# Kernel optimization log

Measured on AMD Instinct MI355X. Metric: run time of the kernel, lower is better.

## Reference

```python
import jax, jax.numpy as jnp
import numpy as np

N = 50000      # nodes
E = 600000     # edges
G = 256        # graphs in batch
HID = 128      # gcn hidden = gcn in = gcn out
EDIM = 16      # edge feature dim
EH = 64        # edge mlp hidden
NL = 4         # gcn layers
MIN_ = 200     # mol feature dim
MH = 256       # mlp hidden
MOUT = 128     # mlp out
PH = 512       # predictor hidden
PIN = HID + MOUT


def setup_inputs() -> dict:
    key = jax.random.key(0)
    ks = jax.random.split(key, 32)
    f = lambda k, s: jax.random.normal(k, s, dtype=jnp.float32)
    p = lambda k, s: 0.05 * jax.random.normal(k, s, dtype=jnp.float32)
    return {
        "x": f(ks[0], (N, HID)),
        "edge_index": jax.random.randint(ks[1], (2, E), 0, N),
        "edge_attr": f(ks[2], (E, EDIM)),
        "batch_index": jnp.sort(jax.random.randint(ks[3], (N,), 0, G)),
        "mol_features": f(ks[4], (G, MIN_)),
        # PDNConv params (stacked over NL layers)
        "conv_lin_W": p(ks[5], (NL, HID, HID)),
        "conv_mW1": p(ks[6], (NL, EDIM, EH)),
        "conv_mb1": p(ks[7], (NL, EH)),
        "conv_mW2": p(ks[8], (NL, EH)),
        "conv_mb2": p(ks[9], (NL,)),
        "conv_bias": p(ks[10], (NL, HID)),
        # dense Linear after each conv
        "gcn_W": p(ks[11], (NL, HID, HID)),
        "gcn_b": p(ks[12], (NL, HID)),
        # mol-feature MLP (n_mlp_layers=3 -> 4 linears)
        "mlp_W0": p(ks[13], (MIN_, MH)), "mlp_b0": p(ks[14], (MH,)),
        "mlp_W1": p(ks[15], (MH, MH)),   "mlp_b1": p(ks[16], (MH,)),
        "mlp_W2": p(ks[17], (MH, MH)),   "mlp_b2": p(ks[18], (MH,)),
        "mlp_W3": p(ks[19], (MH, MOUT)), "mlp_b3": p(ks[20], (MOUT,)),
        # predictor
        "pred_W0": p(ks[21], (PIN, PH)), "pred_b0": p(ks[22], (PH,)),
        "pred_W1": p(ks[23], (PH, PH)),  "pred_b1": p(ks[24], (PH,)),
        "out_W": p(ks[25], (PH, 1)),     "out_b": p(ks[26], (1,)),
    }


def _pdn_conv(h, row, col, edge_attr, lin_W, mW1, mb1, mW2, mb2, bias):
    # edge MLP -> sigmoid gate (PyG PDNConv)
    w = jax.nn.sigmoid(jnp.maximum(edge_attr @ mW1 + mb1, 0.0) @ mW2 + mb2)  # [E]
    # gcn_norm with self loops (fill weight 1.0)
    loop = jnp.arange(N)
    r = jnp.concatenate([row, loop])
    c = jnp.concatenate([col, loop])
    w_all = jnp.concatenate([w, jnp.ones((N,), h.dtype)])
    deg = jax.ops.segment_sum(w_all, c, num_segments=N)
    dinv = jnp.where(deg > 0, jax.lax.rsqrt(deg), 0.0)
    norm = dinv[r] * w_all * dinv[c]                                          # [E+N]
    hl = h @ lin_W                                                            # [N,HID]
    out = jax.ops.segment_sum(norm[:, None] * hl[r], c, num_segments=N)
    return out + bias


def reference(x, edge_index, edge_attr, batch_index, mol_features,
              conv_lin_W, conv_mW1, conv_mb1, conv_mW2, conv_mb2, conv_bias,
              gcn_W, gcn_b,
              mlp_W0, mlp_b0, mlp_W1, mlp_b1, mlp_W2, mlp_b2, mlp_W3, mlp_b3,
              pred_W0, pred_b0, pred_W1, pred_b1, out_W, out_b):
    row, col = edge_index[0], edge_index[1]
    relu = lambda v: jnp.maximum(v, 0.0)

    # GCN stack: PDNConv -> relu(Linear), x NL
    h1 = x
    for i in range(NL):
        h1 = _pdn_conv(h1, row, col, edge_attr, conv_lin_W[i], conv_mW1[i],
                       conv_mb1[i], conv_mW2[i], conv_mb2[i], conv_bias[i])
        h1 = relu(h1 @ gcn_W[i] + gcn_b[i])
    # global mean pool over graphs
    sums = jax.ops.segment_sum(h1, batch_index, num_segments=G)
    cnts = jax.ops.segment_sum(jnp.ones((N,), h1.dtype), batch_index, num_segments=G)
    h1 = sums / jnp.maximum(cnts, 1.0)[:, None]                               # [G,HID]

    # molecular-feature MLP
    h2 = relu(mol_features @ mlp_W0 + mlp_b0)
    h2 = relu(h2 @ mlp_W1 + mlp_b1)
    h2 = relu(h2 @ mlp_W2 + mlp_b2)
    h2 = relu(h2 @ mlp_W3 + mlp_b3)                                           # [G,MOUT]

    h = jnp.concatenate([h1, h2], axis=1)                                     # [G,PIN]
    h = relu(h @ pred_W0 + pred_b0)
    h = relu(h @ pred_W1 + pred_b1)
    return h @ out_W + out_b                                                  # [G,1]
```

## Files before the change

### kernel.cpp

```cpp
#include <hip/hip_runtime.h>
#include <hip/hip_bf16.h>


#define NN 50000
#define EE 600000
#define GG 256
#define HID 128
#define EDIM 16
#define EHID 64
#define NL 4
#define MIN_F 200
#define MH 256
#define MOUT 128
#define PH 512
#define PIN 256
#define SCAN_B 196
#define PCH 8
#define EMB 128

typedef __hip_bfloat16 bf16;
typedef __attribute__((ext_vector_type(8))) short bf16x8;
typedef __attribute__((ext_vector_type(4))) float f32x4;

__device__ __forceinline__ float bfl(unsigned u) { return __uint_as_float(u << 16); }
__device__ __forceinline__ float bfh(unsigned u) { return __uint_as_float(u & 0xffff0000u); }
__device__ __forceinline__ float b2f(bf16 x) { return __bfloat162float(x); }
__device__ __forceinline__ float ldf(const void* p, long i, bool bf) {
  return bf ? __bfloat162float(((const bf16*)p)[i]) : ((const float*)p)[i];
}
__device__ __forceinline__ unsigned short f2bf_bits(float v) {
  bf16 h = __float2bfloat16(v);
  return *reinterpret_cast<unsigned short*>(&h);
}

__global__ void probe_kernel(const unsigned short* __restrict__ xs, int* flag) {
  if (threadIdx.x == 0 && blockIdx.x == 0) {
    int sane = 0;
    for (int i = 0; i < 128; i++) {
      unsigned e = (xs[i] >> 7) & 0xFF;
      if (e >= 96 && e <= 159) sane++;
    }
    *flag = (sane >= 112) ? 1 : 0;
  }
}

__global__ __launch_bounds__(256) void cvt_to_bf16(const void* __restrict__ in,
                                                   unsigned short* __restrict__ outp,
                                                   int n8, const int* __restrict__ flag) {
  bool bf = *flag != 0;
  int i = blockIdx.x * 256 + threadIdx.x;
  if (i >= n8) return;
  if (bf) {
    reinterpret_cast<uint4*>(outp)[i] = reinterpret_cast<const uint4*>(in)[i];
  } else {
    const float4* p = reinterpret_cast<const float4*>(in) + (size_t)i * 2;
    float4 v0 = p[0], v1 = p[1];
    ushort4 a, b;
    a.x = f2bf_bits(v0.x); a.y = f2bf_bits(v0.y);
    a.z = f2bf_bits(v0.z); a.w = f2bf_bits(v0.w);
    b.x = f2bf_bits(v1.x); b.y = f2bf_bits(v1.y);
    b.z = f2bf_bits(v1.z); b.w = f2bf_bits(v1.w);
    reinterpret_cast<ushort4*>(outp)[i * 2] = a;
    reinterpret_cast<ushort4*>(outp)[i * 2 + 1] = b;
  }
}

__global__ __launch_bounds__(256) void cvt_molf(const void* __restrict__ in,
                                                float* __restrict__ outp,
                                                const int* __restrict__ flag) {
  bool bf = *flag != 0;
  int i = blockIdx.x * 256 + threadIdx.x;
  if (i >= GG * 50) return;
  int row = i / 50, c4 = (i % 50) * 4;
  float4 v;
  if (bf) {
    const unsigned short* p = (const unsigned short*)in + (size_t)row * MIN_F + c4;
    uint2 u = *reinterpret_cast<const uint2*>(p);
    v.x = bfl(u.x); v.y = bfh(u.x); v.z = bfl(u.y); v.w = bfh(u.y);
  } else {
    v = *reinterpret_cast<const float4*>((const float*)in + (size_t)row * MIN_F + c4);
  }
  *reinterpret_cast<float4*>(&outp[(size_t)row * 256 + c4]) = v;
}

__global__ __launch_bounds__(256) void prep_fused_w(const void* __restrict__ lin_W,
                                                    const void* __restrict__ gW,
                                                    unsigned short* __restrict__ Wt,
                                                    const int* __restrict__ flag) {
  bool bf = *flag != 0;
  int idx = blockIdx.x * 256 + threadIdx.x;
  if (idx >= 4 * 16384) return;
  int l = idx >> 14;
  int rem = idx & 16383;
  int n = rem >> 7, k = rem & 127;
  float s = 0.f;
  long lb = (long)l * 16384;
  for (int m = 0; m < 128; m++)
    s += ldf(lin_W, lb + (long)k * 128 + m, bf) * ldf(gW, lb + (long)m * 128 + n, bf);
  Wt[idx] = f2bf_bits(s);
}

__global__ __launch_bounds__(128) void prep_fused_b(const void* __restrict__ cbias,
                                                    const void* __restrict__ gW,
                                                    const void* __restrict__ gb,
                                                    float* __restrict__ bprime,
                                                    const int* __restrict__ flag) {
  bool bf = *flag != 0;
  int idx = blockIdx.x * 128 + threadIdx.x;
  if (idx >= NL * HID) return;
  int l = idx >> 7, n = idx & 127;
  float s = ldf(gb, idx, bf);
  long lb = (long)l * 16384;
  for (int k = 0; k < 128; k++)
    s += ldf(cbias, (long)l * 128 + k, bf) * ldf(gW, lb + (long)k * 128 + n, bf);
  bprime[idx] = s;
}

__global__ __launch_bounds__(256) void prep_edge_w(const void* __restrict__ mW1,
                                                   const void* __restrict__ mb1,
                                                   unsigned short* __restrict__ W1t,
                                                   const int* __restrict__ flag) {
  bool bf = *flag != 0;
  int idx = blockIdx.x * 256 + threadIdx.x;
  if (idx >= 256 * 32) return;
  int col = idx >> 5, k = idx & 31;
  float v = 0.f;
  if (k < EDIM) v = ldf(mW1, (long)(col >> 6) * (EDIM * EHID) + (long)k * EHID + (col & 63), bf);
  else if (k == EDIM) v = ldf(mb1, col, bf);
  W1t[idx] = f2bf_bits(v);
}

__global__ __launch_bounds__(256) void prep_tail(
    const void* __restrict__ mlpW0, const void* __restrict__ mlpW1,
    const void* __restrict__ mlpW2, const void* __restrict__ mlpW3,
    const void* __restrict__ predW0, const void* __restrict__ predW1,
    unsigned short* __restrict__ T, const int* __restrict__ flag) {
  bool bf = *flag != 0;
  int idx = blockIdx.x * 256 + threadIdx.x;
  const void* src; int N, Kp, Ksrc, off;
  if      (idx < 65536)  { src = mlpW0;  N = 256; Kp = 256; Ksrc = 200; off = 0; }
  else if (idx < 131072) { src = mlpW1;  N = 256; Kp = 256; Ksrc = 256; off = 65536; }
  else if (idx < 196608) { src = mlpW2;  N = 256; Kp = 256; Ksrc = 256; off = 131072; }
  else if (idx < 229376) { src = mlpW3;  N = 128; Kp = 256; Ksrc = 256; off = 196608; }
  else if (idx < 360448) { src = predW0; N = 512; Kp = 256; Ksrc = 256; off = 229376; }
  else if (idx < 622592) { src = predW1; N = 512; Kp = 512; Ksrc = 512; off = 360448; }
  else return;
  int rem = idx - off;
  int n = rem / Kp, k = rem % Kp;
  float v = (k < Ksrc) ? ldf(src, (long)k * N + n, bf) : 0.f;
  T[idx] = f2bf_bits(v);
}

__global__ __launch_bounds__(256) void count_kernel(const int* __restrict__ ei,
                                                    int* __restrict__ cnt) {
  int e = blockIdx.x * 256 + threadIdx.x;
  if (e >= EE) return;
  int c = ei[EE + e];
  c = min(max(c, 0), NN - 1);
  atomicAdd(&cnt[c], 1);
}

__global__ __launch_bounds__(256) void scan_phase1(const int* __restrict__ cnt,
                                                   int* __restrict__ bsum) {
  __shared__ int red[256];
  int tid = threadIdx.x;
  int i = blockIdx.x * 256 + tid;
  red[tid] = (i < NN) ? cnt[i] : 0;
  __syncthreads();
  for (int off = 128; off > 0; off >>= 1) {
    if (tid < off) red[tid] += red[tid + off];
    __syncthreads();
  }
  if (tid == 0) bsum[blockIdx.x] = red[0];
}

__global__ __launch_bounds__(256) void scan_phase2(int* __restrict__ bsum,
                                                   int* __restrict__ offs) {
  __shared__ int buf[256];
  int tid = threadIdx.x;
  int v = (tid < SCAN_B) ? bsum[tid] : 0;
  buf[tid] = v;
  __syncthreads();
  for (int off = 1; off < 256; off <<= 1) {
    int t = (tid >= off) ? buf[tid - off] : 0;
    __syncthreads();
    buf[tid] += t;
    __syncthreads();
  }
  if (tid < SCAN_B) bsum[tid] = buf[tid] - v;
  if (tid == 255) offs[NN] = buf[255];
}

__global__ __launch_bounds__(256) void scan_phase3(const int* __restrict__ cnt,
                                                   const int* __restrict__ bsum,
                                                   int* __restrict__ offs) {
  __shared__ int buf[256];
  int tid = threadIdx.x;
  int i = blockIdx.x * 256 + tid;
  int v = (i < NN) ? cnt[i] : 0;
  buf[tid] = v;
  __syncthreads();
  for (int off = 1; off < 256; off <<= 1) {
    int t = (tid >= off) ? buf[tid - off] : 0;
    __syncthreads();
    buf[tid] += t;
    __syncthreads();
  }
  if (i < NN) offs[i] = bsum[blockIdx.x] + buf[tid] - v;
}

__global__ __launch_bounds__(256) void fill_kernel(const int* __restrict__ ei,
                                                   const int* __restrict__ offs,
                                                   int* __restrict__ cursor,
                                                   int2* __restrict__ csr_se) {
  int e = blockIdx.x * 256 + threadIdx.x;
  if (e >= EE) return;
  int c = ei[EE + e];
  c = min(max(c, 0), NN - 1);
  int pos = offs[c] + atomicAdd(&cursor[c], 1);
  pos = min(max(pos, 0), EE - 1);
  csr_se[pos] = make_int2(ei[e], e);
}

__global__ __launch_bounds__(256) void edge_mlp_mfma(
    const void* __restrict__ eattr, const unsigned short* __restrict__ W1t,
    const void* __restrict__ mW2, const void* __restrict__ mb2,
    float* __restrict__ w_all4, const int* __restrict__ flag) {
  bool bf = *flag != 0;
  int tid = threadIdx.x;
  int wave = tid >> 6, lane = tid & 63;
  int l15 = lane & 15, quad = lane >> 4;

  bf16x8 afrag[4];
#pragma unroll
  for (int t = 0; t < 4; t++)
    afrag[t] =
        *reinterpret_cast<const bf16x8*>(&W1t[((wave * 4 + t) * 16 + l15) * 32 + quad * 8]);

  float w2v[16];
#pragma unroll
  for (int t = 0; t < 4; t++)
#pragma unroll
    for (int r = 0; r < 4; r++)
      w2v[t * 4 + r] = ldf(mW2, wave * 64 + t * 16 + quad * 4 + r, bf);
  float b2 = ldf(mb2, wave, bf);

  bf16x8 bconst = (bf16x8){0, 0, 0, 0, 0, 0, 0, 0};
  if (quad == 2) bconst[0] = (short)0x3F80;

  int ebase = blockIdx.x * EMB;
  int rowbytes = bf ? EDIM * 2 : EDIM * 4;
  const char* p = (const char*)eattr + (size_t)(ebase + l15) * rowbytes +
                  (size_t)quad * (rowbytes >> 1);
  int fragstep = 16 * rowbytes;

  auto loadb = [&](int fb, const char* pp) -> bf16x8 {
    bf16x8 v = bconst;
    if (quad < 2 && fb < EE) {
      if (bf) {
        v = *reinterpret_cast<const bf16x8*>(pp);
      } else {
        const float4* q = reinterpret_cast<const float4*>(pp);
        float4 v0 = q[0], v1 = q[1];
        v[0] = (short)f2bf_bits(v0.x); v[1] = (short)f2bf_bits(v0.y);
        v[2] = (short)f2bf_bits(v0.z); v[3] = (short)f2bf_bits(v0.w);
        v[4] = (short)f2bf_bits(v1.x); v[5] = (short)f2bf_bits(v1.y);
        v[6] = (short)f2bf_bits(v1.z); v[7] = (short)f2bf_bits(v1.w);
      }
    }
    return v;
  };

  bf16x8 bcur = loadb(ebase, p);
#pragma unroll 2
  for (int f = 0; f < EMB / 16; f++) {
    int fbase = ebase + f * 16;
    p += fragstep;
    bf16x8 bnxt = loadb(fbase + 16, p);
    if (fbase < EE) {
      float s0 = 0.f, s1 = 0.f, s2 = 0.f, s3 = 0.f;
#define DO_T(T, S)                                                            \
  {                                                                           \
    f32x4 acc = __builtin_amdgcn_mfma_f32_16x16x32_bf16(                      \
        afrag[T], bcur, (f32x4){0.f, 0.f, 0.f, 0.f}, 0, 0, 0);                \
    S = fmaf(fmaxf(acc.x, 0.f), w2v[T * 4 + 0], S);                           \
    S = fmaf(fmaxf(acc.y, 0.f), w2v[T * 4 + 1], S);                           \
    S = fmaf(fmaxf(acc.z, 0.f), w2v[T * 4 + 2], S);                           \
    S = fmaf(fmaxf(acc.w, 0.f), w2v[T * 4 + 3], S);                           \
  }
      DO_T(0, s0) DO_T(1, s1) DO_T(2, s2) DO_T(3, s3)
#undef DO_T
      float s = (s0 + s1) + (s2 + s3);
      s += __shfl_xor(s, 16);
      s += __shfl_xor(s, 32);
      if (quad == 0) {
        float g = 1.f / (1.f + __expf(-(s + b2)));
        w_all4[(size_t)(fbase + l15) * 4 + wave] = g;
      }
    }
    bcur = bnxt;
  }
}

__global__ __launch_bounds__(256) void csr_gather(const int2* __restrict__ csr_se,
                                                  const float* __restrict__ w_all4,
                                                  float* __restrict__ csr_val) {
  int k = blockIdx.x * 256 + threadIdx.x;
  if (k >= EE) return;
  int eid = csr_se[k].y;
  eid = min(max(eid, 0), EE - 1);
  float4 w = reinterpret_cast<const float4*>(w_all4)[eid];
  csr_val[k] = w.x;
  csr_val[(size_t)EE + k] = w.y;
  csr_val[2 * (size_t)EE + k] = w.z;
  csr_val[3 * (size_t)EE + k] = w.w;
}

__global__ __launch_bounds__(256) void deg_kernel(const int* __restrict__ offs,
                                                  const float* __restrict__ csr_val,
                                                  float* __restrict__ dinv4) {
  int n = blockIdx.x * 256 + threadIdx.x;
  if (n >= NN) return;
  int s = offs[n], e = offs[n + 1];
  float d0 = 1.f, d1 = 1.f, d2 = 1.f, d3 = 1.f;
  for (int k = s; k < e; k++) {
    d0 += csr_val[k];
    d1 += csr_val[EE + k];
    d2 += csr_val[2 * (size_t)EE + k];
    d3 += csr_val[3 * (size_t)EE + k];
  }
  float4 o;
  o.x = rsqrtf(d0); o.y = rsqrtf(d1); o.z = rsqrtf(d2); o.w = rsqrtf(d3);
  reinterpret_cast<float4*>(dinv4)[n] = o;
}

__global__ __launch_bounds__(256) void csr_scale_kernel(const int2* __restrict__ csr_se,
                                                        const float* __restrict__ dinv4,
                                                        float* __restrict__ csr_val) {
  int k = blockIdx.x * 256 + threadIdx.x;
  if (k >= EE) return;
  int s = csr_se[k].x;
  s = min(max(s, 0), NN - 1);
  float4 d = reinterpret_cast<const float4*>(dinv4)[s];
  csr_val[k] *= d.x;
  csr_val[(size_t)EE + k] *= d.y;
  csr_val[2 * (size_t)EE + k] *= d.z;
  csr_val[3 * (size_t)EE + k] *= d.w;
}

__global__ __launch_bounds__(256) void gemm_nodes_bf16(
    const unsigned short* __restrict__ A16, const unsigned short* __restrict__ Wt,
    const float* __restrict__ bias, unsigned short* __restrict__ out16,
    int relu) {
  __shared__ alignas(16) unsigned short sA[64 * 136];
  __shared__ alignas(16) unsigned short sW[128 * 136];
  int tid = threadIdx.x;
  int rbase = blockIdx.x * 64;

#pragma unroll
  for (int p = 0; p < 8; p++) {
    int idx8 = p * 256 + tid;
    int n = idx8 >> 4, kc = idx8 & 15;
    uint4 v = reinterpret_cast<const uint4*>(Wt)[idx8];
    *reinterpret_cast<uint4*>(&sW[n * 136 + kc * 8]) = v;
  }
#pragma unroll
  for (int p = 0; p < 4; p++) {
    int idx8 = p * 256 + tid;
    int m = idx8 >> 4, kc = idx8 & 15;
    int row = rbase + m;
    uint4 v = make_uint4(0u, 0u, 0u, 0u);
    if (row < NN)
      v = *reinterpret_cast<const uint4*>(&A16[(size_t)row * HID + kc * 8]);
    *reinterpret_cast<uint4*>(&sA[m * 136 + kc * 8]) = v;
  }
  __syncthreads();

  int wave = tid >> 6, lane = tid & 63;
  int l15 = lane & 15, quad = lane >> 4;
  int mstrip = wave * 16;

  f32x4 acc[8];
#pragma unroll
  for (int t = 0; t < 8; t++) acc[t] = (f32x4){0.f, 0.f, 0.f, 0.f};

#pragma unroll
  for (int ks = 0; ks < 4; ks++) {
    int k0 = ks * 32 + quad * 8;
    bf16x8 a = *reinterpret_cast<const bf16x8*>(&sA[(mstrip + l15) * 136 + k0]);
#pragma unroll
    for (int t = 0; t < 8; t++) {
      bf16x8 b = *reinterpret_cast<const bf16x8*>(&sW[(t * 16 + l15) * 136 + k0]);
      acc[t] = __builtin_amdgcn_mfma_f32_16x16x32_bf16(a, b, acc[t], 0, 0, 0);
    }
  }

#pragma unroll
  for (int t = 0; t < 8; t++) {
    int n = t * 16 + l15;
    float bv = bias ? bias[n] : 0.f;
#pragma unroll
    for (int r = 0; r < 4; r++) {
      int row = rbase + mstrip + quad * 4 + r;
      if (row < NN) {
        float o = acc[t][r] + bv;
        if (relu) o = fmaxf(o, 0.f);
        out16[(size_t)row * HID + n] = f2bf_bits(o);
      }
    }
  }
}

__global__ __launch_bounds__(256) void gemm_tail_mfma(
    const float* __restrict__ A, int lda, const unsigned short* __restrict__ Wt,
    int Kp, const void* __restrict__ bias, float* __restrict__ outp, int ldo,
    int relu, const int* __restrict__ flag) {
  __shared__ alignas(16) unsigned short sA[64 * 264];
  __shared__ alignas(16) unsigned short sW[64 * 264];
  int tid = threadIdx.x;
  int rbase = blockIdx.x * 64;
  int nbase = blockIdx.y * 64;
  int wave = tid >> 6, lane = tid & 63;
  int l15 = lane & 15, quad = lane >> 4;
  int mstrip = wave * 16;

  f32x4 acc[4];
#pragma unroll
  for (int t = 0; t < 4; t++) acc[t] = (f32x4){0.f, 0.f, 0.f, 0.f};

  for (int kc = 0; kc < Kp; kc += 256) {
#pragma unroll 4
    for (int p = 0; p < 16; p++) {
      int idx = p * 1024 + tid * 4;
      int m = idx >> 8, k = idx & 255;
      float4 v = *reinterpret_cast<const float4*>(&A[(size_t)(rbase + m) * lda + kc + k]);
      ushort4 b;
      b.x = f2bf_bits(v.x); b.y = f2bf_bits(v.y);
      b.z = f2bf_bits(v.z); b.w = f2bf_bits(v.w);
      *reinterpret_cast<ushort4*>(&sA[m * 264 + k]) = b;
    }
#pragma unroll 4
    for (int p = 0; p < 8; p++) {
      int idx8 = p * 256 + tid;
      int n = idx8 >> 5, kk = (idx8 & 31) * 8;
      uint4 v = *reinterpret_cast<const uint4*>(&Wt[(size_t)(nbase + n) * Kp + kc + kk]);
      *reinterpret_cast<uint4*>(&sW[n * 264 + kk]) = v;
    }
    __syncthreads();
#pragma unroll
    for (int ks = 0; ks < 8; ks++) {
      int k0 = ks * 32 + quad * 8;
      bf16x8 a = *reinterpret_cast<const bf16x8*>(&sA[(mstrip + l15) * 264 + k0]);
#pragma unroll
      for (int nt = 0; nt < 4; nt++) {
        bf16x8 b = *reinterpret_cast<const bf16x8*>(&sW[(nt * 16 + l15) * 264 + k0]);
        acc[nt] = __builtin_amdgcn_mfma_f32_16x16x32_bf16(a, b, acc[nt], 0, 0, 0);
      }
    }
    __syncthreads();
  }

  bool bf = *flag != 0;
#pragma unroll
  for (int nt = 0; nt < 4; nt++) {
    int col = nbase + nt * 16 + l15;
    float bv = ldf(bias, col, bf);
#pragma unroll
    for (int r = 0; r < 4; r++) {
      int row = rbase + mstrip + quad * 4 + r;
      float o = acc[nt][r] + bv;
      if (relu) o = fmaxf(o, 0.f);
      outp[(size_t)row * ldo + col] = o;
    }
  }
}

__global__ __launch_bounds__(64) void aggregate_kernel(
    const unsigned short* __restrict__ h16, const int* __restrict__ offs,
    const int2* __restrict__ csr_se, const float* __restrict__ csr_val,
    const float* __restrict__ dinv4, int layer,
    unsigned short* __restrict__ out16) {
  int n = blockIdx.x;
  int lane = threadIdx.x;
  int grp = lane >> 4;
  int c16 = lane & 15;
  __shared__ int s_src[64];
  __shared__ float s_val[64];
  int start = offs[n], end = offs[n + 1];
  float a0 = 0.f, a1 = 0.f, a2 = 0.f, a3 = 0.f;
  float a4 = 0.f, a5 = 0.f, a6 = 0.f, a7 = 0.f;
  for (int base = start; base < end; base += 64) {
    int k = base + lane;
    if (k < end) {
      s_src[lane] = min(max(csr_se[k].x, 0), NN - 1);
      s_val[lane] = csr_val[k];
    }
    __syncthreads();
    int m = min(64, end - base);
    for (int j = grp; j < m; j += 4) {
      float v = s_val[j];
      uint4 u = *reinterpret_cast<const uint4*>(&h16[(size_t)s_src[j] * HID + c16 * 8]);
      a0 = fmaf(v, bfl(u.x), a0); a1 = fmaf(v, bfh(u.x), a1);
      a2 = fmaf(v, bfl(u.y), a2); a3 = fmaf(v, bfh(u.y), a3);
      a4 = fmaf(v, bfl(u.z), a4); a5 = fmaf(v, bfh(u.z), a5);
      a6 = fmaf(v, bfl(u.w), a6); a7 = fmaf(v, bfh(u.w), a7);
    }
    __syncthreads();
  }
  a0 += __shfl_xor(a0, 16); a1 += __shfl_xor(a1, 16);
  a2 += __shfl_xor(a2, 16); a3 += __shfl_xor(a3, 16);
  a4 += __shfl_xor(a4, 16); a5 += __shfl_xor(a5, 16);
  a6 += __shfl_xor(a6, 16); a7 += __shfl_xor(a7, 16);
  a0 += __shfl_xor(a0, 32); a1 += __shfl_xor(a1, 32);
  a2 += __shfl_xor(a2, 32); a3 += __shfl_xor(a3, 32);
  a4 += __shfl_xor(a4, 32); a5 += __shfl_xor(a5, 32);
  a6 += __shfl_xor(a6, 32); a7 += __shfl_xor(a7, 32);
  if (grp == 0) {
    float dn = dinv4[(size_t)n * 4 + layer];
    float dn2 = dn * dn;
    uint4 su = *reinterpret_cast<const uint4*>(&h16[(size_t)n * HID + c16 * 8]);
    ushort4 o0, o1v;
    o0.x  = f2bf_bits(dn * a0 + dn2 * bfl(su.x));
    o0.y  = f2bf_bits(dn * a1 + dn2 * bfh(su.x));
    o0.z  = f2bf_bits(dn * a2 + dn2 * bfl(su.y));
    o0.w  = f2bf_bits(dn * a3 + dn2 * bfh(su.y));
    o1v.x = f2bf_bits(dn * a4 + dn2 * bfl(su.z));
    o1v.y = f2bf_bits(dn * a5 + dn2 * bfh(su.z));
    o1v.z = f2bf_bits(dn * a6 + dn2 * bfl(su.w));
    o1v.w = f2bf_bits(dn * a7 + dn2 * bfh(su.w));
    *reinterpret_cast<ushort4*>(&out16[(size_t)n * HID + c16 * 8]) = o0;
    *reinterpret_cast<ushort4*>(&out16[(size_t)n * HID + c16 * 8 + 4]) = o1v;
  }
}

__global__ __launch_bounds__(128) void pool_partial(const unsigned short* __restrict__ h16,
                                                    const int* __restrict__ batch,
                                                    float* __restrict__ part) {
  int g = blockIdx.x, chunk = blockIdx.y, c = threadIdx.x;
  int lo = 0, hi = NN;
  while (lo < hi) { int mid = (lo + hi) >> 1; if (batch[mid] < g) lo = mid + 1; else hi = mid; }
  int start = lo;
  hi = NN;
  while (lo < hi) { int mid = (lo + hi) >> 1; if (batch[mid] < g + 1) lo = mid + 1; else hi = mid; }
  int end = lo;
  int len = end - start;
  int per = (len + PCH - 1) / PCH;
  int s = start + chunk * per;
  int e = min(s + per, end);
  float sum = 0.f;
  for (int n = s; n < e; n++) sum += bfl((unsigned)h16[(size_t)n * HID + c]);
  part[((size_t)g * PCH + chunk) * HID + c] = sum;
}

__global__ __launch_bounds__(128) void pool_combine(const float* __restrict__ part,
                                                    const int* __restrict__ batch,
                                                    float* __restrict__ cat) {
  int g = blockIdx.x, c = threadIdx.x;
  int lo = 0, hi = NN;
  while (lo < hi) { int mid = (lo + hi) >> 1; if (batch[mid] < g) lo = mid + 1; else hi = mid; }
  int start = lo;
  hi = NN;
  while (lo < hi) { int mid = (lo + hi) >> 1; if (batch[mid] < g + 1) lo = mid + 1; else hi = mid; }
  int end = lo;
  float s = 0.f;
#pragma unroll
  for (int k = 0; k < PCH; k++) s += part[((size_t)g * PCH + k) * HID + c];
  float cntf = (float)(end - start);
  cat[(size_t)g * PIN + c] = s / fmaxf(cntf, 1.f);
}

__global__ __launch_bounds__(64) void final_kernel(const float* __restrict__ A,
                                                   const void* __restrict__ W,
                                                   const void* __restrict__ b,
                                                   void* __restrict__ outp,
                                                   const int* __restrict__ flag) {
  bool bf = *flag != 0;
  int g = blockIdx.x, lane = threadIdx.x;
  float s = 0.f;
  for (int k = lane; k < PH; k += 64) s = fmaf(A[(size_t)g * PH + k], ldf(W, k, bf), s);
#pragma unroll
  for (int off = 32; off > 0; off >>= 1) s += __shfl_down(s, off);
  if (lane == 0) {
    float r = s + ldf(b, 0, bf);
    if (bf) ((bf16*)outp)[g] = __float2bfloat16(r);
    else    ((float*)outp)[g] = r;
  }
}

extern "C" void kernel_launch(void* const* d_in, const int* in_sizes, int n_in,
                              void* d_out, int out_size, void* d_ws, size_t ws_size,
                              hipStream_t stream) {
  const void* x      = d_in[0];
  const int*  ei     = (const int*)d_in[1];
  const void* eattr  = d_in[2];
  const int*  batch  = (const int*)d_in[3];
  const void* molf   = d_in[4];
  const void* lin_W  = d_in[5];
  const void* mW1    = d_in[6];
  const void* mb1    = d_in[7];
  const void* mW2    = d_in[8];
  const void* mb2    = d_in[9];
  const void* cbias  = d_in[10];
  const void* gW     = d_in[11];
  const void* gb     = d_in[12];
  const void* mlpW0  = d_in[13];
  const void* mlpb0  = d_in[14];
  const void* mlpW1  = d_in[15];
  const void* mlpb1  = d_in[16];
  const void* mlpW2  = d_in[17];
  const void* mlpb2  = d_in[18];
  const void* mlpW3  = d_in[19];
  const void* mlpb3  = d_in[20];
  const void* predW0 = d_in[21];
  const void* predb0 = d_in[22];
  const void* predW1 = d_in[23];
  const void* predb1 = d_in[24];
  const void* outW   = d_in[25];
  const void* outb   = d_in[26];

  char* base = (char*)d_ws;
  size_t off = 0;
  auto alloc = [&](size_t bytes) -> char* {
    char* p = base + off;
    off = (off + bytes + 255) & ~(size_t)255;
    return p;
  };
  unsigned short* h16  = (unsigned short*)alloc((size_t)NN * HID * 2);
  unsigned short* t16  = (unsigned short*)alloc((size_t)NN * HID * 2);
  float* dinv4    = (float*)alloc((size_t)NN * 4 * 4);
  int*   cnt      = (int*)alloc((size_t)NN * 4);
  int*   offs     = (int*)alloc((size_t)(NN + 1) * 4);
  int*   cursor   = (int*)alloc((size_t)NN * 4);
  int*   bsum     = (int*)alloc((size_t)256 * 4);
  int2*  csr_se   = (int2*)alloc((size_t)EE * 8);
  float* csr_val  = (float*)alloc((size_t)NL * EE * 4);
  float* w_all4   = (float*)alloc((size_t)EE * 4 * 4);
  unsigned short* Wt    = (unsigned short*)alloc((size_t)NL * HID * HID * 2);
  float* bprime   = (float*)alloc((size_t)NL * HID * 4);
  unsigned short* tailW = (unsigned short*)alloc((size_t)622592 * 2);
  unsigned short* edgeW = (unsigned short*)alloc((size_t)256 * 32 * 2);
  int*   flag     = (int*)alloc(256);
  float* part     = (float*)alloc((size_t)GG * PCH * HID * 4);
  float* molf32   = (float*)alloc((size_t)GG * 256 * 4);
  float* m0       = (float*)alloc((size_t)GG * MH * 4);
  float* m1       = (float*)alloc((size_t)GG * MH * 4);
  float* cat      = (float*)alloc((size_t)GG * PIN * 4);
  float* p0       = (float*)alloc((size_t)GG * PH * 4);
  float* p1       = (float*)alloc((size_t)GG * PH * 4);

  hipMemsetAsync(cnt, 0, (size_t)NN * 4, stream);
  hipMemsetAsync(cursor, 0, (size_t)NN * 4, stream);
  hipMemsetAsync(molf32, 0, (size_t)GG * 256 * 4, stream);

  probe_kernel<<<1, 64, 0, stream>>>((const unsigned short*)x, flag);

  prep_fused_w<<<256, 256, 0, stream>>>(lin_W, gW, Wt, flag);
  prep_fused_b<<<NL, 128, 0, stream>>>(cbias, gW, gb, bprime, flag);
  prep_tail<<<(622592 + 255) / 256, 256, 0, stream>>>(mlpW0, mlpW1, mlpW2, mlpW3,
                                                      predW0, predW1, tailW, flag);
  prep_edge_w<<<32, 256, 0, stream>>>(mW1, mb1, edgeW, flag);

  {
    int n8 = NN * HID / 8;
    cvt_to_bf16<<<(n8 + 255) / 256, 256, 0, stream>>>(x, h16, n8, flag);
  }
  edge_mlp_mfma<<<(EE + EMB - 1) / EMB, 256, 0, stream>>>(eattr, edgeW, mW2, mb2,
                                                          w_all4, flag);
  count_kernel<<<(EE + 255) / 256, 256, 0, stream>>>(ei, cnt);
  scan_phase1<<<SCAN_B, 256, 0, stream>>>(cnt, bsum);
  scan_phase2<<<1, 256, 0, stream>>>(bsum, offs);
  scan_phase3<<<SCAN_B, 256, 0, stream>>>(cnt, bsum, offs);
  fill_kernel<<<(EE + 255) / 256, 256, 0, stream>>>(ei, offs, cursor, csr_se);
  csr_gather<<<(EE + 255) / 256, 256, 0, stream>>>(csr_se, w_all4, csr_val);
  deg_kernel<<<(NN + 255) / 256, 256, 0, stream>>>(offs, csr_val, dinv4);
  csr_scale_kernel<<<(EE + 255) / 256, 256, 0, stream>>>(csr_se, dinv4, csr_val);

  const int gemm_blocks = (NN + 63) / 64;
  for (int l = 0; l < NL; l++) {
    aggregate_kernel<<<NN, 64, 0, stream>>>(h16, offs, csr_se,
                                            csr_val + (size_t)l * EE, dinv4, l, t16);
    gemm_nodes_bf16<<<gemm_blocks, 256, 0, stream>>>(
        t16, Wt + (size_t)l * HID * HID, bprime + (size_t)l * HID, h16, 1);
  }

  pool_partial<<<dim3(GG, PCH), 128, 0, stream>>>(h16, batch, part);
  pool_combine<<<GG, 128, 0, stream>>>(part, batch, cat);

  cvt_molf<<<(GG * 50 + 255) / 256, 256, 0, stream>>>(molf, molf32, flag);
  gemm_tail_mfma<<<dim3(4, 4), 256, 0, stream>>>(molf32, 256, tailW + 0,      256, mlpb0, m0, 256, 1, flag);
  gemm_tail_mfma<<<dim3(4, 4), 256, 0, stream>>>(m0,     256, tailW + 65536,  256, mlpb1, m1, 256, 1, flag);
  gemm_tail_mfma<<<dim3(4, 4), 256, 0, stream>>>(m1,     256, tailW + 131072, 256, mlpb2, m0, 256, 1, flag);
  gemm_tail_mfma<<<dim3(4, 2), 256, 0, stream>>>(m0,     256, tailW + 196608, 256, mlpb3, cat + MOUT, 256, 1, flag);

  gemm_tail_mfma<<<dim3(4, 8), 256, 0, stream>>>(cat, 256, tailW + 229376, 256, predb0, p0, 512, 1, flag);
  gemm_tail_mfma<<<dim3(4, 8), 256, 0, stream>>>(p0,  512, tailW + 360448, 512, predb1, p1, 512, 1, flag);
  final_kernel<<<GG, 64, 0, stream>>>(p1, outW, outb, d_out, flag);
}
```

Before: 573.6 us.

## Pack CSR source and per-layer edge weights into 32-byte records, drop gather kernel

The fill kernel now writes each CSR entry as a 32-byte record holding the source index and all four layer gate values, read from w_all4 at fill time. This removes the separate csr_gather kernel and the eid indirection. The degree, scale and aggregate kernels read from these records instead of the separate planar arrays. The trade-off is that each aggregate pass now loads 20 bytes per edge with strided access instead of 12 bytes, and the record buffer is 32 bytes per edge.

```diff
diff --git a/kernel.cpp b/kernel.cpp
--- a/kernel.cpp
+++ b/kernel.cpp
@@ -212,14 +212,19 @@
 __global__ __launch_bounds__(256) void fill_kernel(const int* __restrict__ ei,
                                                    const int* __restrict__ offs,
                                                    int* __restrict__ cursor,
-                                                   int2* __restrict__ csr_se) {
+                                                   const float4* __restrict__ w_all4,
+                                                   char* __restrict__ csr_rec) {
   int e = blockIdx.x * 256 + threadIdx.x;
   if (e >= EE) return;
   int c = ei[EE + e];
   c = min(max(c, 0), NN - 1);
+  int src = min(max(ei[e], 0), NN - 1);
+  float4 g = w_all4[e];
   int pos = offs[c] + atomicAdd(&cursor[c], 1);
   pos = min(max(pos, 0), EE - 1);
-  csr_se[pos] = make_int2(ei[e], e);
+  char* r = csr_rec + (size_t)pos * 32;
+  *reinterpret_cast<int*>(r) = src;
+  *reinterpret_cast<float4*>(r + 16) = g;
 }
 
 __global__ __launch_bounds__(256) void edge_mlp_mfma(
@@ -302,50 +307,34 @@
   }
 }
 
-__global__ __launch_bounds__(256) void csr_gather(const int2* __restrict__ csr_se,
-                                                  const float* __restrict__ w_all4,
-                                                  float* __restrict__ csr_val) {
-  int k = blockIdx.x * 256 + threadIdx.x;
-  if (k >= EE) return;
-  int eid = csr_se[k].y;
-  eid = min(max(eid, 0), EE - 1);
-  float4 w = reinterpret_cast<const float4*>(w_all4)[eid];
-  csr_val[k] = w.x;
-  csr_val[(size_t)EE + k] = w.y;
-  csr_val[2 * (size_t)EE + k] = w.z;
-  csr_val[3 * (size_t)EE + k] = w.w;
-}
-
 __global__ __launch_bounds__(256) void deg_kernel(const int* __restrict__ offs,
-                                                  const float* __restrict__ csr_val,
+                                                  const char* __restrict__ csr_rec,
                                                   float* __restrict__ dinv4) {
   int n = blockIdx.x * 256 + threadIdx.x;
   if (n >= NN) return;
   int s = offs[n], e = offs[n + 1];
   float d0 = 1.f, d1 = 1.f, d2 = 1.f, d3 = 1.f;
   for (int k = s; k < e; k++) {
-    d0 += csr_val[k];
-    d1 += csr_val[EE + k];
-    d2 += csr_val[2 * (size_t)EE + k];
-    d3 += csr_val[3 * (size_t)EE + k];
+    float4 g = *reinterpret_cast<const float4*>(csr_rec + (size_t)k * 32 + 16);
+    d0 += g.x; d1 += g.y; d2 += g.z; d3 += g.w;
   }
   float4 o;
   o.x = rsqrtf(d0); o.y = rsqrtf(d1); o.z = rsqrtf(d2); o.w = rsqrtf(d3);
   reinterpret_cast<float4*>(dinv4)[n] = o;
 }
 
-__global__ __launch_bounds__(256) void csr_scale_kernel(const int2* __restrict__ csr_se,
-                                                        const float* __restrict__ dinv4,
-                                                        float* __restrict__ csr_val) {
+__global__ __launch_bounds__(256) void csr_scale_kernel(char* __restrict__ csr_rec,
+                                                        const float* __restrict__ dinv4) {
   int k = blockIdx.x * 256 + threadIdx.x;
   if (k >= EE) return;
-  int s = csr_se[k].x;
+  char* r = csr_rec + (size_t)k * 32;
+  int s = *reinterpret_cast<const int*>(r);
   s = min(max(s, 0), NN - 1);
   float4 d = reinterpret_cast<const float4*>(dinv4)[s];
-  csr_val[k] *= d.x;
-  csr_val[(size_t)EE + k] *= d.y;
-  csr_val[2 * (size_t)EE + k] *= d.z;
-  csr_val[3 * (size_t)EE + k] *= d.w;
+  float4* gp = reinterpret_cast<float4*>(r + 16);
+  float4 g = *gp;
+  g.x *= d.x; g.y *= d.y; g.z *= d.z; g.w *= d.w;
+  *gp = g;
 }
 
 __global__ __launch_bounds__(256) void gemm_nodes_bf16(
@@ -477,9 +466,8 @@
 
 __global__ __launch_bounds__(64) void aggregate_kernel(
     const unsigned short* __restrict__ h16, const int* __restrict__ offs,
-    const int2* __restrict__ csr_se, const float* __restrict__ csr_val,
-    const float* __restrict__ dinv4, int layer,
-    unsigned short* __restrict__ out16) {
+    const char* __restrict__ csr_rec, const float* __restrict__ dinv4,
+    int layer, unsigned short* __restrict__ out16) {
   int n = blockIdx.x;
   int lane = threadIdx.x;
   int grp = lane >> 4;
@@ -492,8 +480,12 @@
   for (int base = start; base < end; base += 64) {
     int k = base + lane;
     if (k < end) {
-      s_src[lane] = min(max(csr_se[k].x, 0), NN - 1);
-      s_val[lane] = csr_val[k];
+      const char* r = csr_rec + (size_t)k * 32;
+      int sv = *reinterpret_cast<const int*>(r);
+      float4 g = *reinterpret_cast<const float4*>(r + 16);
+      float v = (layer == 0) ? g.x : (layer == 1) ? g.y : (layer == 2) ? g.z : g.w;
+      s_src[lane] = min(max(sv, 0), NN - 1);
+      s_val[lane] = v;
     }
     __syncthreads();
     int m = min(64, end - base);
@@ -632,8 +624,7 @@
   int*   offs     = (int*)alloc((size_t)(NN + 1) * 4);
   int*   cursor   = (int*)alloc((size_t)NN * 4);
   int*   bsum     = (int*)alloc((size_t)256 * 4);
-  int2*  csr_se   = (int2*)alloc((size_t)EE * 8);
-  float* csr_val  = (float*)alloc((size_t)NL * EE * 4);
+  char*  csr_rec  = alloc((size_t)EE * 32);
   float* w_all4   = (float*)alloc((size_t)EE * 4 * 4);
   unsigned short* Wt    = (unsigned short*)alloc((size_t)NL * HID * HID * 2);
   float* bprime   = (float*)alloc((size_t)NL * HID * 4);
@@ -670,15 +661,14 @@
   scan_phase1<<<SCAN_B, 256, 0, stream>>>(cnt, bsum);
   scan_phase2<<<1, 256, 0, stream>>>(bsum, offs);
   scan_phase3<<<SCAN_B, 256, 0, stream>>>(cnt, bsum, offs);
-  fill_kernel<<<(EE + 255) / 256, 256, 0, stream>>>(ei, offs, cursor, csr_se);
-  csr_gather<<<(EE + 255) / 256, 256, 0, stream>>>(csr_se, w_all4, csr_val);
-  deg_kernel<<<(NN + 255) / 256, 256, 0, stream>>>(offs, csr_val, dinv4);
-  csr_scale_kernel<<<(EE + 255) / 256, 256, 0, stream>>>(csr_se, dinv4, csr_val);
+  fill_kernel<<<(EE + 255) / 256, 256, 0, stream>>>(ei, offs, cursor,
+                                                    (const float4*)w_all4, csr_rec);
+  deg_kernel<<<(NN + 255) / 256, 256, 0, stream>>>(offs, csr_rec, dinv4);
+  csr_scale_kernel<<<(EE + 255) / 256, 256, 0, stream>>>(csr_rec, dinv4);
 
   const int gemm_blocks = (NN + 63) / 64;
   for (int l = 0; l < NL; l++) {
-    aggregate_kernel<<<NN, 64, 0, stream>>>(h16, offs, csr_se,
-                                            csr_val + (size_t)l * EE, dinv4, l, t16);
+    aggregate_kernel<<<NN, 64, 0, stream>>>(h16, offs, csr_rec, dinv4, l, t16);
     gemm_nodes_bf16<<<gemm_blocks, 256, 0, stream>>>(
         t16, Wt + (size_t)l * HID * HID, bprime + (size_t)l * HID, h16, 1);
   }
```

After: 567.2 us. About the same (-1.1%).
